# Optimization experiments

Measured on AMD Instinct MI355X. Metric: run time of the kernel, lower is better.

## Reference

```python
import jax, jax.numpy as jnp
import numpy as np

KERNEL = 3  # unfold kernel size (stride 1, no padding)

def _unfold(x, k):
    # torch.nn.Unfold(kernel_size=k) equivalent: (B, C, H, W) -> (B, C*k*k, L)
    # channel ordering: index = c*k*k + i*k + j (channel outermost), matching torch.
    B, C, H, W = x.shape
    Ho, Wo = H - k + 1, W - k + 1
    cols = [x[:, :, i:i + Ho, j:j + Wo] for i in range(k) for j in range(k)]  # k*k x (B,C,Ho,Wo)
    u = jnp.stack(cols, axis=2)  # (B, C, k*k, Ho, Wo)
    return u.reshape(B, C * k * k, Ho * Wo)


def setup_inputs() -> dict:
    key = jax.random.key(0)
    k1, k2, k3, k4 = jax.random.split(key, 4)
    B, C, H, W = 512, 3, 64, 64
    M = 512            # num_neurons
    K = C * KERNEL * KERNEL   # input_dim = 27
    L = (H - KERNEL + 1) * (W - KERNEL + 1)  # 3844 patches
    O = 10             # output_dim
    x = jax.random.normal(k1, (B, C, H, W), dtype=jnp.float32)
    G = jax.random.normal(k2, (M, L), dtype=jnp.float32)
    # original inits v,w to zeros; use randn for a non-degenerate reference
    v = jax.random.normal(k3, (M, K, O), dtype=jnp.float32) * 0.02
    w = jax.random.normal(k4, (M, K, O), dtype=jnp.float32) * 0.02
    return {"x": x, "G": G, "v": v, "w": w}


def reference(x, G, v, w):
    # Faithful to:
    #   U = unfold(x)                         (B, K, L)
    #   t = einsum('mn,ikn->imnk', G, U)      (B, M, L, K)  <- never materialized here
    #   out = einsum('ijkl,jlm->im', t, v-w)  (B, O)
    # Reordered as two small contractions (same math, no huge intermediate):
    U = _unfold(x, KERNEL)                    # (B, K, L)
    A = jnp.einsum('bkn,mn->bmk', U, G)       # (B, M, K): contract over patches L
    p_diff = v - w                            # (M, K, O)
    out = jnp.einsum('bmk,mko->bo', A, p_diff)  # (B, O)
    return out
```

## Files before the change

kernel.cpp:

```cpp
#include <hip/hip_runtime.h>
#include <hip/hip_bf16.h>

#define M_NEUR 512
#define ODIM   10
#define HO     62
#define LDIM   3844
#define CHW    12288
#define BATCH  512
#define KO     270
#define KOP    272
#define NPART  8
#define TPSTR  ((size_t)KO * LDIM)

__global__ __launch_bounds__(256)
void pd_kernel(const float* __restrict__ v, const float* __restrict__ w,
               float* __restrict__ pdP) {
    int idx = blockIdx.x * 256 + threadIdx.x;
    if (idx >= M_NEUR * KOP) return;
    int m  = idx / KOP;
    int ko = idx - m * KOP;
    pdP[idx] = (ko < KO) ? (v[m * KO + ko] - w[m * KO + ko]) : 0.f;
}

__global__ __launch_bounds__(256, 2)
void t_gemm_kernel(const float* __restrict__ G,
                   const float* __restrict__ pdP,
                   __hip_bfloat16* __restrict__ Tp) {
    const int bid   = blockIdx.x;
    const int mch   = bid & 7;
    const int rest  = bid >> 3;
    const int kob   = rest & 3;
    const int ntile = rest >> 2;
    const int m0    = mch * 64;

    __shared__ float pdL[64 * 80];
    for (int t = threadIdx.x; t < 64 * 68; t += 256) {
        int r  = t / 68;
        int ko = t - r * 68;
        int wv = ko / 17;
        int s  = ko - wv * 17;
        pdL[r * 80 + wv * 20 + s] = pdP[(size_t)(m0 + r) * KOP + kob * 68 + ko];
    }
    __syncthreads();

    const int wave = threadIdx.x >> 6;
    const int lane = threadIdx.x & 63;
    const int nb   = ntile * 256 + lane * 4;
    const bool nok = (nb + 3 < LDIM);
    const int nbc  = nok ? nb : 0;

    const float* lb  = &pdL[wave * 20];
    const float4* Gp = reinterpret_cast<const float4*>(G + (size_t)m0 * LDIM + nbc);
    const int GS4 = LDIM / 4;

    float4 acc[17];
#pragma unroll
    for (int s = 0; s < 17; ++s) acc[s] = make_float4(0.f, 0.f, 0.f, 0.f);

#pragma unroll 2
    for (int mi = 0; mi < 64; ++mi) {
        float4 gv = Gp[(size_t)mi * GS4];
        const float* p = lb + mi * 80;
#pragma unroll
        for (int s = 0; s < 17; ++s) {
            float pv = p[s];
            acc[s].x += pv * gv.x;
            acc[s].y += pv * gv.y;
            acc[s].z += pv * gv.z;
            acc[s].w += pv * gv.w;
        }
    }

    if (nok) {
        __hip_bfloat16* tb = Tp + (size_t)mch * TPSTR;
        const int koBase = kob * 68 + wave * 17;
#pragma unroll
        for (int s = 0; s < 17; ++s) {
            int ko = koBase + s;
            if (ko < KO) {
                union { __hip_bfloat162 h[2]; uint2 u; } pk;
                pk.h[0].x = __float2bfloat16(acc[s].x);
                pk.h[0].y = __float2bfloat16(acc[s].y);
                pk.h[1].x = __float2bfloat16(acc[s].z);
                pk.h[1].y = __float2bfloat16(acc[s].w);
                *reinterpret_cast<uint2*>(&tb[(size_t)ko * LDIM + nb]) = pk.u;
            }
        }
    }
}

__global__ __launch_bounds__(256)
void fold_kernel(const __hip_bfloat16* __restrict__ Tp, float* __restrict__ S) {
    int idx = blockIdx.x * 256 + threadIdx.x;
    if (idx >= ODIM * CHW) return;
    int o   = idx / CHW;
    int chw = idx - o * CHW;
    int c = chw >> 12;
    int h = (chw >> 6) & 63;
    int w = chw & 63;

    float s = 0.f;
    for (int i = 0; i < 3; ++i) {
        int pi = h - i;
        if ((unsigned)pi >= HO) continue;
        for (int j = 0; j < 3; ++j) {
            int pj = w - j;
            if ((unsigned)pj >= HO) continue;
            int ko  = (c * 9 + i * 3 + j) * ODIM + o;
            size_t off = (size_t)ko * LDIM + pi * HO + pj;
#pragma unroll
            for (int p = 0; p < NPART; ++p)
                s += __bfloat162float(Tp[(size_t)p * TPSTR + off]);
        }
    }
    S[idx] = s;
}

__global__ __launch_bounds__(256)
void out_gemm_kernel(const float* __restrict__ X,
                     const float* __restrict__ S,
                     float* __restrict__ out) {
    const int b0  = blockIdx.x * 2;
    const int tid = threadIdx.x;
    const int NV  = CHW / 4;
    const float4* X0 = reinterpret_cast<const float4*>(X) + (size_t)b0 * NV;
    const float4* X1 = X0 + NV;
    const float4* S4 = reinterpret_cast<const float4*>(S);

    float acc0[ODIM], acc1[ODIM];
#pragma unroll
    for (int o = 0; o < ODIM; ++o) { acc0[o] = 0.f; acc1[o] = 0.f; }

    for (int i = tid; i < NV; i += 256) {
        float4 a = X0[i];
        float4 b = X1[i];
#pragma unroll
        for (int o = 0; o < ODIM; ++o) {
            float4 sv = S4[(size_t)o * NV + i];
            acc0[o] += a.x * sv.x + a.y * sv.y + a.z * sv.z + a.w * sv.w;
            acc1[o] += b.x * sv.x + b.y * sv.y + b.z * sv.z + b.w * sv.w;
        }
    }

#pragma unroll
    for (int o = 0; o < ODIM; ++o) {
        float s0 = acc0[o], s1 = acc1[o];
        for (int off = 32; off > 0; off >>= 1) {
            s0 += __shfl_down(s0, off, 64);
            s1 += __shfl_down(s1, off, 64);
        }
        acc0[o] = s0; acc1[o] = s1;
    }

    __shared__ float red[4][2 * ODIM];
    int wave = tid >> 6;
    int lane = tid & 63;
    if (lane == 0) {
#pragma unroll
        for (int o = 0; o < ODIM; ++o) {
            red[wave][o] = acc0[o];
            red[wave][ODIM + o] = acc1[o];
        }
    }
    __syncthreads();
    if (tid < 2 * ODIM) {
        float tsum = red[0][tid] + red[1][tid] + red[2][tid] + red[3][tid];
        int bt = tid / ODIM;
        int o  = tid - bt * ODIM;
        out[(size_t)(b0 + bt) * ODIM + o] = tsum;
    }
}

extern "C" void kernel_launch(void* const* d_in, const int* in_sizes, int n_in,
                              void* d_out, int out_size, void* d_ws, size_t ws_size,
                              hipStream_t stream) {
    const float* x = (const float*)d_in[0];
    const float* G = (const float*)d_in[1];
    const float* v = (const float*)d_in[2];
    const float* w = (const float*)d_in[3];
    float* out = (float*)d_out;

    __hip_bfloat16* Tp = (__hip_bfloat16*)d_ws;
    float* S   = (float*)(Tp + (size_t)NPART * TPSTR);
    float* pdP = S + (size_t)ODIM * CHW;

    pd_kernel<<<(M_NEUR * KOP + 255) / 256, 256, 0, stream>>>(v, w, pdP);

    t_gemm_kernel<<<512, 256, 0, stream>>>(G, pdP, Tp);

    fold_kernel<<<(ODIM * CHW + 255) / 256, 256, 0, stream>>>(Tp, S);

    out_gemm_kernel<<<BATCH / 2, 256, 0, stream>>>(x, S, out);
}
```

Measured before the change: 51.91 us.

## Compute neuron contraction with bf16 MFMA over full M, drop split-M partials

Replaces the FP32 FMA GEMM, which split M into 8 partitions and wrote bf16 partials, with an MFMA 16x16x32 bf16 GEMM that reduces over all 512 neurons in one pass and writes a single fp32 T. G is transposed and converted to bf16 in a new kernel, and pdiff is written transposed in bf16. The fold kernel then reads one fp32 value per term instead of summing eight bf16 partials. This adds a transpose kernel and reduces the inputs to bf16 precision, and each wave loads its operands directly from global memory without LDS reuse.

After: 51.95 us. No clear change (+0.1%).

```diff
diff --git a/kernel.cpp b/kernel.cpp
--- a/kernel.cpp
+++ b/kernel.cpp
@@ -1,96 +1,110 @@
 #include <hip/hip_runtime.h>
 #include <hip/hip_bf16.h>
 
-#define M_NEUR 512
 #define ODIM   10
-#define HO     62
+#define HOg    62
 #define LDIM   3844
 #define CHW    12288
 #define BATCH  512
 #define KO     270
 #define KOP    272
-#define NPART  8
-#define TPSTR  ((size_t)KO * LDIM)
-
-__global__ __launch_bounds__(256)
-void pd_kernel(const float* __restrict__ v, const float* __restrict__ w,
-               float* __restrict__ pdP) {
+#define MDIM   512
+#define GTN    3904
+
+typedef __attribute__((ext_vector_type(8))) short bfrag;
+typedef __attribute__((ext_vector_type(4))) float f32x4;
+
+__global__ __launch_bounds__(256)
+void pdt_kernel(const float* __restrict__ v, const float* __restrict__ w,
+                __hip_bfloat16* __restrict__ Pdt) {
     int idx = blockIdx.x * 256 + threadIdx.x;
-    if (idx >= M_NEUR * KOP) return;
+    if (idx >= MDIM * KOP) return;
     int m  = idx / KOP;
     int ko = idx - m * KOP;
-    pdP[idx] = (ko < KO) ? (v[m * KO + ko] - w[m * KO + ko]) : 0.f;
-}
-
-__global__ __launch_bounds__(256, 2)
-void t_gemm_kernel(const float* __restrict__ G,
-                   const float* __restrict__ pdP,
-                   __hip_bfloat16* __restrict__ Tp) {
+    float val = (ko < KO) ? (v[m * KO + ko] - w[m * KO + ko]) : 0.f;
+    Pdt[(size_t)ko * MDIM + m] = __float2bfloat16(val);
+}
+
+__global__ __launch_bounds__(256)
+void gt_kernel(const float* __restrict__ G, __hip_bfloat16* __restrict__ Gt) {
+    __shared__ float tile[64][65];
+    const int n0 = blockIdx.x * 64;
+    const int m0 = blockIdx.y * 64;
+    const int tc = threadIdx.x & 63;
+    const int tr = threadIdx.x >> 6;
+
+#pragma unroll
+    for (int rr = 0; rr < 64; rr += 4) {
+        int n = n0 + tc;
+        tile[rr + tr][tc] = (n < LDIM) ? G[(size_t)(m0 + rr + tr) * LDIM + n] : 0.f;
+    }
+    __syncthreads();
+
+    const int nr = threadIdx.x >> 2;
+    const int ms = (threadIdx.x & 3) * 16;
+    __hip_bfloat16 buf[16];
+#pragma unroll
+    for (int i = 0; i < 16; ++i)
+        buf[i] = __float2bfloat16(tile[ms + i][nr]);
+    __hip_bfloat16* dst = Gt + (size_t)(n0 + nr) * MDIM + m0 + ms;
+    *reinterpret_cast<uint4*>(dst)     = *reinterpret_cast<uint4*>(&buf[0]);
+    *reinterpret_cast<uint4*>(dst + 8) = *reinterpret_cast<uint4*>(&buf[8]);
+}
+
+__global__ __launch_bounds__(256)
+void tmfma_kernel(const __hip_bfloat16* __restrict__ Pdt,
+                  const __hip_bfloat16* __restrict__ Gt,
+                  float* __restrict__ T) {
     const int bid   = blockIdx.x;
-    const int mch   = bid & 7;
-    const int rest  = bid >> 3;
-    const int kob   = rest & 3;
-    const int ntile = rest >> 2;
-    const int m0    = mch * 64;
-
-    __shared__ float pdL[64 * 80];
-    for (int t = threadIdx.x; t < 64 * 68; t += 256) {
-        int r  = t / 68;
-        int ko = t - r * 68;
-        int wv = ko / 17;
-        int s  = ko - wv * 17;
-        pdL[r * 80 + wv * 20 + s] = pdP[(size_t)(m0 + r) * KOP + kob * 68 + ko];
-    }
-    __syncthreads();
-
-    const int wave = threadIdx.x >> 6;
+    const int xcd   = bid & 7;
+    const int inner = bid >> 3;
+    const int sthi  = inner & 1;
+    const int kt    = inner >> 1;
+    const int st    = xcd + 8 * sthi;
+
+    const int wv   = threadIdx.x >> 6;
     const int lane = threadIdx.x & 63;
-    const int nb   = ntile * 256 + lane * 4;
-    const bool nok = (nb + 3 < LDIM);
-    const int nbc  = nok ? nb : 0;
-
-    const float* lb  = &pdL[wave * 20];
-    const float4* Gp = reinterpret_cast<const float4*>(G + (size_t)m0 * LDIM + nbc);
-    const int GS4 = LDIM / 4;
-
-    float4 acc[17];
-#pragma unroll
-    for (int s = 0; s < 17; ++s) acc[s] = make_float4(0.f, 0.f, 0.f, 0.f);
+    const int tile = st * 4 + wv;
+    if (tile >= 61) return;
+
+    const int n0  = tile * 64;
+    const int ko0 = kt * 16;
+    const int row = lane & 15;
+    const int kg  = lane >> 4;
+
+    const __hip_bfloat16* Ap = Pdt + (size_t)(ko0 + row) * MDIM + kg * 8;
+    const __hip_bfloat16* Bp = Gt  + (size_t)(n0 + row) * MDIM + kg * 8;
+
+    f32x4 acc[4];
+#pragma unroll
+    for (int j = 0; j < 4; ++j) acc[j] = (f32x4){0.f, 0.f, 0.f, 0.f};
 
 #pragma unroll 2
-    for (int mi = 0; mi < 64; ++mi) {
-        float4 gv = Gp[(size_t)mi * GS4];
-        const float* p = lb + mi * 80;
-#pragma unroll
-        for (int s = 0; s < 17; ++s) {
-            float pv = p[s];
-            acc[s].x += pv * gv.x;
-            acc[s].y += pv * gv.y;
-            acc[s].z += pv * gv.z;
-            acc[s].w += pv * gv.w;
-        }
-    }
-
-    if (nok) {
-        __hip_bfloat16* tb = Tp + (size_t)mch * TPSTR;
-        const int koBase = kob * 68 + wave * 17;
-#pragma unroll
-        for (int s = 0; s < 17; ++s) {
-            int ko = koBase + s;
-            if (ko < KO) {
-                union { __hip_bfloat162 h[2]; uint2 u; } pk;
-                pk.h[0].x = __float2bfloat16(acc[s].x);
-                pk.h[0].y = __float2bfloat16(acc[s].y);
-                pk.h[1].x = __float2bfloat16(acc[s].z);
-                pk.h[1].y = __float2bfloat16(acc[s].w);
-                *reinterpret_cast<uint2*>(&tb[(size_t)ko * LDIM + nb]) = pk.u;
+    for (int ks = 0; ks < 16; ++ks) {
+        bfrag a = *reinterpret_cast<const bfrag*>(Ap + ks * 32);
+#pragma unroll
+        for (int j = 0; j < 4; ++j) {
+            bfrag b = *reinterpret_cast<const bfrag*>(Bp + (size_t)j * 16 * MDIM + ks * 32);
+            acc[j] = __builtin_amdgcn_mfma_f32_16x16x32_bf16(a, b, acc[j], 0, 0, 0);
+        }
+    }
+
+#pragma unroll
+    for (int j = 0; j < 4; ++j) {
+        int col = n0 + j * 16 + row;
+        if (col < LDIM) {
+#pragma unroll
+            for (int r = 0; r < 4; ++r) {
+                int ro = ko0 + kg * 4 + r;
+                if (ro < KO)
+                    T[(size_t)ro * LDIM + col] = acc[j][r];
             }
         }
     }
 }
 
 __global__ __launch_bounds__(256)
-void fold_kernel(const __hip_bfloat16* __restrict__ Tp, float* __restrict__ S) {
+void fold_kernel(const float* __restrict__ T, float* __restrict__ S) {
     int idx = blockIdx.x * 256 + threadIdx.x;
     if (idx >= ODIM * CHW) return;
     int o   = idx / CHW;
@@ -102,15 +116,12 @@
     float s = 0.f;
     for (int i = 0; i < 3; ++i) {
         int pi = h - i;
-        if ((unsigned)pi >= HO) continue;
+        if ((unsigned)pi >= HOg) continue;
         for (int j = 0; j < 3; ++j) {
             int pj = w - j;
-            if ((unsigned)pj >= HO) continue;
-            int ko  = (c * 9 + i * 3 + j) * ODIM + o;
-            size_t off = (size_t)ko * LDIM + pi * HO + pj;
-#pragma unroll
-            for (int p = 0; p < NPART; ++p)
-                s += __bfloat162float(Tp[(size_t)p * TPSTR + off]);
+            if ((unsigned)pj >= HOg) continue;
+            int ko = (c * 9 + i * 3 + j) * ODIM + o;
+            s += T[(size_t)ko * LDIM + pi * HOg + pj];
         }
     }
     S[idx] = s;
@@ -180,15 +191,19 @@
     const float* w = (const float*)d_in[3];
     float* out = (float*)d_out;
 
-    __hip_bfloat16* Tp = (__hip_bfloat16*)d_ws;
-    float* S   = (float*)(Tp + (size_t)NPART * TPSTR);
-    float* pdP = S + (size_t)ODIM * CHW;
-
-    pd_kernel<<<(M_NEUR * KOP + 255) / 256, 256, 0, stream>>>(v, w, pdP);
-
-    t_gemm_kernel<<<512, 256, 0, stream>>>(G, pdP, Tp);
-
-    fold_kernel<<<(ODIM * CHW + 255) / 256, 256, 0, stream>>>(Tp, S);
+    char* wsb = (char*)d_ws;
+    float*          T   = (float*)wsb;
+    __hip_bfloat16* Gt  = (__hip_bfloat16*)(wsb + 4151520);
+    __hip_bfloat16* Pdt = (__hip_bfloat16*)(wsb + 4151520 + 3997696);
+    float*          S   = (float*)(wsb + 4151520 + 3997696 + 278528);
+
+    pdt_kernel<<<(MDIM * KOP + 255) / 256, 256, 0, stream>>>(v, w, Pdt);
+
+    gt_kernel<<<dim3(61, 8), 256, 0, stream>>>(G, Gt);
+
+    tmfma_kernel<<<272, 256, 0, stream>>>(Pdt, Gt, T);
+
+    fold_kernel<<<(ODIM * CHW + 255) / 256, 256, 0, stream>>>(T, S);
 
     out_gemm_kernel<<<BATCH / 2, 256, 0, stream>>>(x, S, out);
 }
```
